# Kernel tuning notes

Hardware: AMD Instinct MI355X
Metric: run time of the kernel (lower is better)

## Reference

```python
import jax, jax.numpy as jnp
import numpy as np

S = 16384      # imwidth * imheight = 128 * 128
RANK = 64
N = 8          # number of TT cores; 6 middle cores


def setup_inputs() -> dict:
    key = jax.random.key(0)
    k1, k2, k3, k4 = jax.random.split(key, 4)
    z = jax.random.normal(k1, (S,), dtype=jnp.float32)
    # TT cores: first (1, s, r), middle (N-2, r, s, r), last (r, s, 1)
    tt_first = jax.random.normal(k2, (1, S, RANK), dtype=jnp.float32) / np.float32(np.sqrt(S))
    tt_mid = jax.random.normal(k3, (N - 2, RANK, S, RANK), dtype=jnp.float32) / np.float32(np.sqrt(S))
    tt_last = jax.random.normal(k4, (RANK, S, 1), dtype=jnp.float32) / np.float32(np.sqrt(S))
    return {"z": z, "tt_first": tt_first, "tt_mid": tt_mid, "tt_last": tt_last}


def reference(z, tt_first, tt_mid, tt_last):
    # V[k] = z contracted with core k over the s axis -> (d1, d2)
    V_mid = jnp.einsum('s,kasb->kab', z, tt_mid)   # (N-2, r, r)
    V_last = jnp.einsum('s,asb->ab', z, tt_last)   # (r, 1)
    f = tt_first[0]                                 # (s, r)
    # strictly sequential chain of small matmuls: f = f @ V[1] @ ... @ V[N-2]
    def step(f, Vk):
        return f @ Vk, None
    f, _ = jax.lax.scan(step, f, V_mid)             # (s, r)
    f = f @ V_last                                  # (s, 1)
    return f.reshape(-1)
```

## Files before the change

### kernel.cpp

```cpp
#include <hip/hip_runtime.h>

#define SDIM 16384
#define RANK 64
#define NMID 6
#define NCHUNK 8
#define CHUNK_LEN (SDIM / NCHUNK)

__global__ __launch_bounds__(256) void k_vmid_partial(
    const float* __restrict__ z, const float* __restrict__ tt_mid,
    float* __restrict__ part) {
  const int idx = blockIdx.x;
  const int c  = idx & (NCHUNK - 1);
  const int ka = idx / NCHUNK;
  const float* __restrict__ src =
      tt_mid + ((size_t)ka * SDIM + (size_t)c * CHUNK_LEN) * RANK;
  const float* __restrict__ zz = z + (size_t)c * CHUNK_LEN;

  const int b8  = threadIdx.x & 7;
  const int row = threadIdx.x >> 3;

  float4 acc0 = {0.f, 0.f, 0.f, 0.f};
  float4 acc1 = {0.f, 0.f, 0.f, 0.f};
#pragma unroll 4
  for (int s = row; s < CHUNK_LEN; s += 32) {
    const float w = zz[s];
    const float4* p =
        reinterpret_cast<const float4*>(src + (size_t)s * RANK + b8 * 8);
    const float4 v0 = p[0];
    const float4 v1 = p[1];
    acc0.x += w * v0.x; acc0.y += w * v0.y; acc0.z += w * v0.z; acc0.w += w * v0.w;
    acc1.x += w * v1.x; acc1.y += w * v1.y; acc1.z += w * v1.z; acc1.w += w * v1.w;
  }

  __shared__ float4 lds[512];
  lds[threadIdx.x * 2]     = acc0;
  lds[threadIdx.x * 2 + 1] = acc1;
  __syncthreads();
  if (threadIdx.x < 16) {
    float4 sum = {0.f, 0.f, 0.f, 0.f};
    for (int r = 0; r < 32; ++r) {
      const float4 t = lds[r * 16 + threadIdx.x];
      sum.x += t.x; sum.y += t.y; sum.z += t.z; sum.w += t.w;
    }
    *reinterpret_cast<float4*>(
        part + ((size_t)ka * NCHUNK + c) * RANK + threadIdx.x * 4) = sum;
  }
}

__global__ __launch_bounds__(256) void k_vlast(
    const float* __restrict__ z, const float* __restrict__ tt_last,
    float* __restrict__ vlast) {
  const int a = blockIdx.x;
  const float* __restrict__ src = tt_last + (size_t)a * SDIM;
  float acc = 0.f;
  for (int i = threadIdx.x; i < SDIM / 4; i += 256) {
    const float4 v = *reinterpret_cast<const float4*>(src + i * 4);
    const float4 w = *reinterpret_cast<const float4*>(z + i * 4);
    acc += v.x * w.x + v.y * w.y + v.z * w.z + v.w * w.w;
  }
  __shared__ float lds[256];
  lds[threadIdx.x] = acc;
  __syncthreads();
  for (int off = 128; off > 0; off >>= 1) {
    if (threadIdx.x < off) lds[threadIdx.x] += lds[threadIdx.x + off];
    __syncthreads();
  }
  if (threadIdx.x == 0) vlast[a] = lds[0];
}

__global__ __launch_bounds__(64) void k_fold(
    const float* __restrict__ part, float* __restrict__ V) {
  const int ka = blockIdx.x;
  const int b  = threadIdx.x;
  float s = 0.f;
#pragma unroll
  for (int c = 0; c < NCHUNK; ++c)
    s += part[((size_t)ka * NCHUNK + c) * RANK + b];
  V[(size_t)ka * RANK + b] = s;
}

__global__ __launch_bounds__(256) void k_chain(
    const float* __restrict__ V, const float* __restrict__ vlast,
    float* __restrict__ u) {
  __shared__ float su[RANK];
  __shared__ float snew[RANK];
  __shared__ float red[256];
  if (threadIdx.x < RANK) su[threadIdx.x] = vlast[threadIdx.x];
  __syncthreads();

  const int a = threadIdx.x >> 2;
  const int t = threadIdx.x & 3;
  for (int k = NMID - 1; k >= 0; --k) {
    const float* __restrict__ Vk =
        V + (size_t)k * RANK * RANK + (size_t)a * RANK + t * 16;
    float s = 0.f;
#pragma unroll
    for (int b = 0; b < 16; ++b) s += Vk[b] * su[t * 16 + b];
    red[threadIdx.x] = s;
    __syncthreads();
    if (t == 0)
      snew[a] = red[a * 4] + red[a * 4 + 1] + red[a * 4 + 2] + red[a * 4 + 3];
    __syncthreads();
    if (threadIdx.x < RANK) su[threadIdx.x] = snew[threadIdx.x];
    __syncthreads();
  }
  if (threadIdx.x < RANK) u[threadIdx.x] = su[threadIdx.x];
}

__global__ __launch_bounds__(256) void k_out(
    const float* __restrict__ tt_first, const float* __restrict__ u,
    float* __restrict__ out) {
  const int r = blockIdx.x * 16 + (threadIdx.x >> 4);
  const int j = threadIdx.x & 15;
  const float4 v =
      *reinterpret_cast<const float4*>(tt_first + (size_t)r * RANK + j * 4);
  const float4 w = *reinterpret_cast<const float4*>(u + j * 4);
  float s = v.x * w.x + v.y * w.y + v.z * w.z + v.w * w.w;
  s += __shfl_xor(s, 1, 16);
  s += __shfl_xor(s, 2, 16);
  s += __shfl_xor(s, 4, 16);
  s += __shfl_xor(s, 8, 16);
  if (j == 0) out[r] = s;
}

extern "C" void kernel_launch(void* const* d_in, const int* in_sizes, int n_in,
                              void* d_out, int out_size, void* d_ws,
                              size_t ws_size, hipStream_t stream) {
  const float* z        = (const float*)d_in[0];
  const float* tt_first = (const float*)d_in[1];
  const float* tt_mid   = (const float*)d_in[2];
  const float* tt_last  = (const float*)d_in[3];
  float* out = (float*)d_out;
  float* ws  = (float*)d_ws;

  float* part  = ws;
  float* V     = part + (size_t)NMID * RANK * NCHUNK * RANK;
  float* vlast = V + (size_t)NMID * RANK * RANK;
  float* u     = vlast + RANK;

  k_vmid_partial<<<NMID * RANK * NCHUNK, 256, 0, stream>>>(z, tt_mid, part);
  k_vlast<<<RANK, 256, 0, stream>>>(z, tt_last, vlast);
  k_fold<<<NMID * RANK, 64, 0, stream>>>(part, V);
  k_chain<<<1, 256, 0, stream>>>(V, vlast, u);
  k_out<<<SDIM / 16, 256, 0, stream>>>(tt_first, u, out);
}
```

Measured before the change: 283.0 us.

## Merge vmid/vlast contractions and fuse chain into output kernel

Combines the tt_mid and tt_last contractions into a single launch with block-index dispatch. It also merges the sequential chain and the output GEMV: each of the 1024 output blocks recomputes the 64x64 chain redundantly in LDS, so the single-block chain kernel and the u buffer go away. This removes two launches and one serialized single-block kernel, at the cost of redundant chain work and extra V reads in every output block.

```diff
diff --git a/kernel.cpp b/kernel.cpp
--- a/kernel.cpp
+++ b/kernel.cpp
@@ -5,67 +5,69 @@
 #define NMID 6
 #define NCHUNK 8
 #define CHUNK_LEN (SDIM / NCHUNK)
+#define VMID_BLOCKS (NMID * RANK * NCHUNK)
 
-__global__ __launch_bounds__(256) void k_vmid_partial(
+__global__ __launch_bounds__(256) void k_contract(
     const float* __restrict__ z, const float* __restrict__ tt_mid,
-    float* __restrict__ part) {
-  const int idx = blockIdx.x;
-  const int c  = idx & (NCHUNK - 1);
-  const int ka = idx / NCHUNK;
-  const float* __restrict__ src =
-      tt_mid + ((size_t)ka * SDIM + (size_t)c * CHUNK_LEN) * RANK;
-  const float* __restrict__ zz = z + (size_t)c * CHUNK_LEN;
+    const float* __restrict__ tt_last, float* __restrict__ part,
+    float* __restrict__ vlast) {
+  if (blockIdx.x < VMID_BLOCKS) {
+    const int idx = blockIdx.x;
+    const int c  = idx & (NCHUNK - 1);
+    const int ka = idx / NCHUNK;
+    const float* __restrict__ src =
+        tt_mid + ((size_t)ka * SDIM + (size_t)c * CHUNK_LEN) * RANK;
+    const float* __restrict__ zz = z + (size_t)c * CHUNK_LEN;
 
-  const int b8  = threadIdx.x & 7;
-  const int row = threadIdx.x >> 3;
+    const int b8  = threadIdx.x & 7;
+    const int row = threadIdx.x >> 3;
 
-  float4 acc0 = {0.f, 0.f, 0.f, 0.f};
-  float4 acc1 = {0.f, 0.f, 0.f, 0.f};
+    float4 acc0 = {0.f, 0.f, 0.f, 0.f};
+    float4 acc1 = {0.f, 0.f, 0.f, 0.f};
 #pragma unroll 4
-  for (int s = row; s < CHUNK_LEN; s += 32) {
-    const float w = zz[s];
-    const float4* p =
-        reinterpret_cast<const float4*>(src + (size_t)s * RANK + b8 * 8);
-    const float4 v0 = p[0];
-    const float4 v1 = p[1];
-    acc0.x += w * v0.x; acc0.y += w * v0.y; acc0.z += w * v0.z; acc0.w += w * v0.w;
-    acc1.x += w * v1.x; acc1.y += w * v1.y; acc1.z += w * v1.z; acc1.w += w * v1.w;
+    for (int s = row; s < CHUNK_LEN; s += 32) {
+      const float w = zz[s];
+      const float4* p =
+          reinterpret_cast<const float4*>(src + (size_t)s * RANK + b8 * 8);
+      const float4 v0 = p[0];
+      const float4 v1 = p[1];
+      acc0.x += w * v0.x; acc0.y += w * v0.y;
+      acc0.z += w * v0.z; acc0.w += w * v0.w;
+      acc1.x += w * v1.x; acc1.y += w * v1.y;
+      acc1.z += w * v1.z; acc1.w += w * v1.w;
+    }
+
+    __shared__ float4 lds[512];
+    lds[threadIdx.x * 2]     = acc0;
+    lds[threadIdx.x * 2 + 1] = acc1;
+    __syncthreads();
+    if (threadIdx.x < 16) {
+      float4 sum = {0.f, 0.f, 0.f, 0.f};
+      for (int r = 0; r < 32; ++r) {
+        const float4 t = lds[r * 16 + threadIdx.x];
+        sum.x += t.x; sum.y += t.y; sum.z += t.z; sum.w += t.w;
+      }
+      *reinterpret_cast<float4*>(
+          part + ((size_t)ka * NCHUNK + c) * RANK + threadIdx.x * 4) = sum;
+    }
+  } else {
+    const int a = blockIdx.x - VMID_BLOCKS;
+    const float* __restrict__ src = tt_last + (size_t)a * SDIM;
+    float acc = 0.f;
+    for (int i = threadIdx.x; i < SDIM / 4; i += 256) {
+      const float4 v = *reinterpret_cast<const float4*>(src + i * 4);
+      const float4 w = *reinterpret_cast<const float4*>(z + i * 4);
+      acc += v.x * w.x + v.y * w.y + v.z * w.z + v.w * w.w;
+    }
+    __shared__ float red[256];
+    red[threadIdx.x] = acc;
+    __syncthreads();
+    for (int off = 128; off > 0; off >>= 1) {
+      if (threadIdx.x < off) red[threadIdx.x] += red[threadIdx.x + off];
+      __syncthreads();
+    }
+    if (threadIdx.x == 0) vlast[a] = red[0];
   }
-
-  __shared__ float4 lds[512];
-  lds[threadIdx.x * 2]     = acc0;
-  lds[threadIdx.x * 2 + 1] = acc1;
-  __syncthreads();
-  if (threadIdx.x < 16) {
-    float4 sum = {0.f, 0.f, 0.f, 0.f};
-    for (int r = 0; r < 32; ++r) {
-      const float4 t = lds[r * 16 + threadIdx.x];
-      sum.x += t.x; sum.y += t.y; sum.z += t.z; sum.w += t.w;
-    }
-    *reinterpret_cast<float4*>(
-        part + ((size_t)ka * NCHUNK + c) * RANK + threadIdx.x * 4) = sum;
-  }
-}
-
-__global__ __launch_bounds__(256) void k_vlast(
-    const float* __restrict__ z, const float* __restrict__ tt_last,
-    float* __restrict__ vlast) {
-  const int a = blockIdx.x;
-  const float* __restrict__ src = tt_last + (size_t)a * SDIM;
-  float acc = 0.f;
-  for (int i = threadIdx.x; i < SDIM / 4; i += 256) {
-    const float4 v = *reinterpret_cast<const float4*>(src + i * 4);
-    const float4 w = *reinterpret_cast<const float4*>(z + i * 4);
-    acc += v.x * w.x + v.y * w.y + v.z * w.z + v.w * w.w;
-  }
-  __shared__ float lds[256];
-  lds[threadIdx.x] = acc;
-  __syncthreads();
-  for (int off = 128; off > 0; off >>= 1) {
-    if (threadIdx.x < off) lds[threadIdx.x] += lds[threadIdx.x + off];
-    __syncthreads();
-  }
-  if (threadIdx.x == 0) vlast[a] = lds[0];
 }
 
 __global__ __launch_bounds__(64) void k_fold(
@@ -79,9 +81,9 @@
   V[(size_t)ka * RANK + b] = s;
 }
 
-__global__ __launch_bounds__(256) void k_chain(
+__global__ __launch_bounds__(256) void k_chain_out(
     const float* __restrict__ V, const float* __restrict__ vlast,
-    float* __restrict__ u) {
+    const float* __restrict__ tt_first, float* __restrict__ out) {
   __shared__ float su[RANK];
   __shared__ float snew[RANK];
   __shared__ float red[256];
@@ -104,17 +106,12 @@
     if (threadIdx.x < RANK) su[threadIdx.x] = snew[threadIdx.x];
     __syncthreads();
   }
-  if (threadIdx.x < RANK) u[threadIdx.x] = su[threadIdx.x];
-}
 
-__global__ __launch_bounds__(256) void k_out(
-    const float* __restrict__ tt_first, const float* __restrict__ u,
-    float* __restrict__ out) {
   const int r = blockIdx.x * 16 + (threadIdx.x >> 4);
   const int j = threadIdx.x & 15;
   const float4 v =
       *reinterpret_cast<const float4*>(tt_first + (size_t)r * RANK + j * 4);
-  const float4 w = *reinterpret_cast<const float4*>(u + j * 4);
+  const float4 w = *reinterpret_cast<const float4*>(su + j * 4);
   float s = v.x * w.x + v.y * w.y + v.z * w.z + v.w * w.w;
   s += __shfl_xor(s, 1, 16);
   s += __shfl_xor(s, 2, 16);
@@ -136,11 +133,8 @@
   float* part  = ws;
   float* V     = part + (size_t)NMID * RANK * NCHUNK * RANK;
   float* vlast = V + (size_t)NMID * RANK * RANK;
-  float* u     = vlast + RANK;
 
-  k_vmid_partial<<<NMID * RANK * NCHUNK, 256, 0, stream>>>(z, tt_mid, part);
-  k_vlast<<<RANK, 256, 0, stream>>>(z, tt_last, vlast);
+  k_contract<<<VMID_BLOCKS + RANK, 256, 0, stream>>>(z, tt_mid, tt_last, part, vlast);
   k_fold<<<NMID * RANK, 64, 0, stream>>>(part, V);
-  k_chain<<<1, 256, 0, stream>>>(V, vlast, u);
-  k_out<<<SDIM / 16, 256, 0, stream>>>(tt_first, u, out);
+  k_chain_out<<<SDIM / 16, 256, 0, stream>>>(V, vlast, tt_first, out);
 }
```

New measurement: 275.8 us, median of 2. 2.5% less time.
